# Optimization experiments

Hardware: AMD Instinct MI355X
Metric: run time of the kernel (lower is better)

Reference implementation:

```python
import jax, jax.numpy as jnp
import numpy as np

N = 65536   # voxels
K = 27      # 3x3x3 kernel offsets
LOG_P = float(np.log(101.0))  # Hmax = log(num img channels)
EPS_BN = 1e-5


def bn(x, p):
    # p: [4, C] = (gamma, beta, running_mean, running_var); eval-mode batchnorm
    g, b, m, v = p[0], p[1], p[2], p[3]
    return g * (x - m) * jax.lax.rsqrt(v + EPS_BN) + b


def spconv(x, nbr, W):
    # sparse 3^3 conv as gather-GEMM: x [N,Cin], nbr [N,K] int, W [K,Cin,Cout]
    g = x[nbr]                       # [N, K, Cin] irregular gather
    return jnp.einsum('nkc,kcd->nd', g, W)


def setup_inputs() -> dict:
    key = jax.random.key(0)
    ks = jax.random.split(key, 24)
    inp = {
        'feats': jax.random.uniform(ks[0], (N, 105), dtype=jnp.float32),
        'nbr1': jax.random.randint(ks[1], (N, K), 0, N, dtype=jnp.int32),
        'nbr2': jax.random.randint(ks[2], (N, K), 0, N, dtype=jnp.int32),
        'w_rgb': jax.random.normal(ks[3], (4, 32), jnp.float32) * 0.1,
        'b_rgb': jax.random.normal(ks[4], (32,), jnp.float32) * 0.1,
        'bn_rgb': jax.random.uniform(ks[5], (4, 32), dtype=jnp.float32),
        'w_img': jax.random.normal(ks[6], (101, 32), jnp.float32) * 0.1,
        'b_img': jax.random.normal(ks[7], (32,), jnp.float32) * 0.1,
        'bn_img': jax.random.uniform(ks[8], (4, 32), dtype=jnp.float32),
        'w_e1': jax.random.normal(ks[9], (K, 64, 96), jnp.float32) * 0.05,
        'w_e2': jax.random.normal(ks[10], (K, 96, 96), jnp.float32) * 0.05,
        'bn_e1': jax.random.uniform(ks[11], (4, 96), dtype=jnp.float32),
        'bn_e2': jax.random.uniform(ks[12], (4, 96), dtype=jnp.float32),
        'w_lab': jax.random.normal(ks[13], (96, 19), jnp.float32) * 0.1,
        'w_unlab': jax.random.normal(ks[14], (5, 96, 5), jnp.float32) * 0.1,
        'w_over': jax.random.normal(ks[15], (5, 96, 15), jnp.float32) * 0.1,
        'w_clip1': jax.random.normal(ks[16], (96, 256), jnp.float32) * 0.1,
        'b_clip1': jax.random.normal(ks[17], (256,), jnp.float32) * 0.1,
        'bn_clip': jax.random.uniform(ks[18], (4, 256), dtype=jnp.float32),
        'w_clip2': jax.random.normal(ks[19], (256, 512), jnp.float32) * 0.1,
        'b_clip2': jax.random.normal(ks[20], (512,), jnp.float32) * 0.1,
    }
    return inp


def reference(feats, nbr1, nbr2, w_rgb, b_rgb, bn_rgb, w_img, b_img, bn_img,
              w_e1, w_e2, bn_e1, bn_e2, w_lab, w_unlab, w_over,
              w_clip1, b_clip1, bn_clip, w_clip2, b_clip2):
    rgbi = feats[:, :4]
    p = feats[:, 4:]
    # entropy gate (computed under no_grad in the original)
    p_safe = jnp.clip(p, 1e-12, None)
    H = -(p_safe * jnp.log(p_safe)).sum(axis=1, keepdims=True)
    w = jax.lax.stop_gradient(1.0 - H / LOG_P)
    p_gate = p * w  # eval mode: no dropout
    # 1x1 sparse convs = per-voxel matmuls
    rgb32 = jax.nn.relu(bn(rgbi @ w_rgb + b_rgb, bn_rgb))
    img32 = jax.nn.relu(bn(p_gate @ w_img + b_img, bn_img))
    x = jnp.concatenate([rgb32, img32], axis=1)  # [N, 64]
    # encoder: gather-GEMM sparse 3^3 convs (MinkUNet body pattern), 64->96->96
    x = jax.nn.relu(bn(spconv(x, nbr1, w_e1), bn_e1))
    x = jax.nn.relu(bn(spconv(x, nbr2, w_e2), bn_e2))  # [N, 96] = feats
    # prototype heads (1x1 convs, bias-free)
    logits_lab = x @ w_lab                                 # [N, 19]
    logits_unlab = jnp.einsum('nc,hcp->hnp', x, w_unlab)   # [5, N, 5]
    logits_over = jnp.einsum('nc,hcp->hnp', x, w_over)     # [5, N, 15]
    # clip projector
    h = jax.nn.relu(bn(x @ w_clip1 + b_clip1, bn_clip))
    clip_feats = h @ w_clip2 + b_clip2                     # [N, 512]
    return (logits_lab, logits_unlab, logits_over, x, clip_feats)
```

## Files before the change

kernel.cpp:

```cpp
#include <hip/hip_runtime.h>
#include <math.h>

#define NNODES 65536
#define KNBR 27
#define EPS_BN 1e-5f
#define LOG_P 4.6151205168412597f

typedef float f32x4 __attribute__((ext_vector_type(4)));
typedef short s16x8 __attribute__((ext_vector_type(8)));

__device__ __forceinline__ unsigned short f2bf(float f) {
    union { float f; unsigned int u; } v; v.f = f;
    unsigned int u = v.u;
    unsigned int r = (u + 0x7fffu + ((u >> 16) & 1u)) >> 16;
    return (unsigned short)r;
}

__device__ __forceinline__ void gload16(const void* g, void* l) {
    __builtin_amdgcn_global_load_lds(
        (const __attribute__((address_space(1))) void*)g,
        (__attribute__((address_space(3))) void*)l, 16, 0, 0);
}

__global__ __launch_bounds__(256) void prep_w_kernel(
    const float* __restrict__ W, unsigned short* __restrict__ wpre, int CIN, int NCH)
{
    const int idx = blockIdx.x * 256 + threadIdx.x;
    const int total = KNBR * 96 * NCH * 8;
    if (idx >= total) return;
    const int e  = idx & 7;
    const int t1 = idx >> 3;
    const int ci = t1 % NCH;
    const int t2 = t1 / NCH;
    const int r  = t2 % 96;
    const int k  = t2 / 96;
    const int cc  = ci ^ (r & (NCH - 1));
    const int cin = cc * 8 + e;
    float v = (cin < CIN) ? W[((size_t)k * CIN + cin) * 96 + r] : 0.f;
    wpre[idx] = f2bf(v);
}

__global__ __launch_bounds__(256) void prep_wc1h_kernel(
    const float* __restrict__ w_clip1, const float* __restrict__ w_lab,
    const float* __restrict__ w_unlab, const float* __restrict__ w_over,
    unsigned short* __restrict__ out)
{
    const int idx = blockIdx.x * 256 + threadIdx.x;
    if (idx >= 3 * 384 * 32) return;
    const int e   = idx & 7;
    const int p2  = (idx >> 3) & 3;
    const int col = (idx >> 5) % 384;
    const int kt  = (idx >> 5) / 384;
    const int cin = (kt * 4 + (p2 ^ ((col >> 2) & 3))) * 8 + e;
    float v;
    if (col < 256)      v = w_clip1[(size_t)cin * 256 + col];
    else if (col < 275) v = w_lab[(size_t)cin * 19 + (col - 256)];
    else if (col < 300) { int jj = col - 275, hh = jj / 5,  p = jj - hh * 5;  v = w_unlab[((size_t)hh * 96 + cin) * 5  + p]; }
    else if (col < 375) { int jj = col - 300, hh = jj / 15, p = jj - hh * 15; v = w_over [((size_t)hh * 96 + cin) * 15 + p]; }
    else v = 0.f;
    out[idx] = f2bf(v);
}

__global__ __launch_bounds__(256) void prep_wc2_kernel(
    const float* __restrict__ w_clip2, unsigned short* __restrict__ out)
{
    const int idx = blockIdx.x * 256 + threadIdx.x;
    const int e   = idx & 7;
    const int p2  = (idx >> 3) & 3;
    const int col = (idx >> 5) & 511;
    const int kt  = idx >> 14;
    const int cin = (kt * 4 + (p2 ^ ((col >> 2) & 3))) * 8 + e;
    out[idx] = f2bf(w_clip2[(size_t)cin * 512 + col]);
}

__global__ __launch_bounds__(256) void stage1_kernel(
    const float* __restrict__ feats,
    const float* __restrict__ w_rgb, const float* __restrict__ b_rgb, const float* __restrict__ bn_rgb,
    const float* __restrict__ w_img, const float* __restrict__ b_img, const float* __restrict__ bn_img,
    unsigned short* __restrict__ x64b)
{
    __shared__ float s_f[4][106];
    const int wid  = threadIdx.x >> 6;
    const int lane = threadIdx.x & 63;
    const int n = blockIdx.x * 4 + wid;
    const float* fr = feats + (size_t)n * 105;
    for (int i = lane; i < 105; i += 64) s_f[wid][i] = fr[i];
    __syncthreads();

    float s = 0.f;
    for (int i = lane; i < 101; i += 64) {
        float pv = s_f[wid][4 + i];
        float ps = fmaxf(pv, 1e-12f);
        s += ps * logf(ps);
    }
    #pragma unroll
    for (int off = 32; off > 0; off >>= 1) s += __shfl_xor(s, off, 64);
    const float wgt = 1.0f + s * (1.0f / LOG_P);

    if (lane < 32) {
        const int j = lane;
        float acc = b_rgb[j];
        #pragma unroll
        for (int c = 0; c < 4; ++c) acc += s_f[wid][c] * w_rgb[c*32 + j];
        float y = bn_rgb[j] * (acc - bn_rgb[64+j]) * rsqrtf(bn_rgb[96+j] + EPS_BN) + bn_rgb[32+j];
        x64b[(size_t)n*64 + j] = f2bf(fmaxf(y, 0.f));
    } else {
        const int j = lane - 32;
        float acc = 0.f;
        for (int c = 0; c < 101; ++c) acc += s_f[wid][4+c] * w_img[c*32 + j];
        acc = acc * wgt + b_img[j];
        float y = bn_img[j] * (acc - bn_img[64+j]) * rsqrtf(bn_img[96+j] + EPS_BN) + bn_img[32+j];
        x64b[(size_t)n*64 + 32 + j] = f2bf(fmaxf(y, 0.f));
    }
}

template<int CIN, bool OUTBF>
__global__ __launch_bounds__(256, 2) void spconv_mfma(
    const char* __restrict__ xinb,
    const int*  __restrict__ nbr,
    const char* __restrict__ wpre,
    const float* __restrict__ bnp,
    float* __restrict__ outf,
    unsigned short* __restrict__ outb)
{
    constexpr int KT   = CIN / 32;
    constexpr int NCH  = (CIN == 96) ? 16 : 8;
    constexpr int CM   = NCH - 1;
    constexpr int ROWB = NCH * 16;
    constexpr int STG  = (96 * ROWB) / 4096;

    __shared__ int s_nbr[128 * KNBR];
    __shared__ __align__(16) char s_b[2][96 * ROWB];

    const int t   = threadIdx.x;
    const int wid = t >> 6;
    const int l   = t & 63;
    const int l15 = l & 15;
    const int l4  = l >> 4;
    const int n0  = blockIdx.x * 128;

    for (int i = t; i < 128 * KNBR; i += 256) s_nbr[i] = nbr[(size_t)n0 * KNBR + i];

    f32x4 acc[2][6];
    #pragma unroll
    for (int mt = 0; mt < 2; ++mt)
        #pragma unroll
        for (int nt = 0; nt < 6; ++nt) acc[mt][nt] = (f32x4){0.f, 0.f, 0.f, 0.f};

    s16x8 a0[2][KT], a1[2][KT], a2r[2][KT];

#define STAGE(kk) do {                                                         \
    const char* _src = wpre + (size_t)(kk) * (96 * ROWB);                      \
    char* _dst = &s_b[(kk) & 1][0];                                            \
    _Pragma("unroll")                                                          \
    for (int _i = 0; _i < STG; ++_i)                                           \
        gload16(_src + _i * 4096 + t * 16, _dst + _i * 4096 + (wid << 10));    \
    asm volatile("" ::: "memory");                                             \
} while (0)

#define PRE(areg, kk) do {                                                     \
    _Pragma("unroll")                                                          \
    for (int _mt = 0; _mt < 2; ++_mt) {                                        \
        const int _nb = s_nbr[(wid * 32 + _mt * 16 + l15) * KNBR + (kk)];      \
        const char* _rp = xinb + (size_t)_nb * (CIN * 2) + (l4 << 4);          \
        _Pragma("unroll")                                                      \
        for (int _kt = 0; _kt < KT; ++_kt)                                     \
            areg[_mt][_kt] = *(const s16x8*)(_rp + _kt * 64);                  \
    }                                                                          \
} while (0)

#define COMP(areg, kk) do {                                                    \
    const char* _bb = &s_b[(kk) & 1][0];                                       \
    _Pragma("unroll")                                                          \
    for (int _kt = 0; _kt < KT; ++_kt) {                                       \
        s16x8 _bf[6];                                                          \
        _Pragma("unroll")                                                      \
        for (int _nt = 0; _nt < 6; ++_nt) {                                    \
            const int _row = _nt * 16 + l15;                                   \
            const int _c   = _kt * 4 + l4;                                     \
            _bf[_nt] = *(const s16x8*)(_bb + _row * ROWB + ((_c ^ (_row & CM)) << 4)); \
        }                                                                      \
        _Pragma("unroll")                                                      \
        for (int _nt = 0; _nt < 6; ++_nt) {                                    \
            acc[0][_nt] = __builtin_amdgcn_mfma_f32_16x16x32_bf16(areg[0][_kt], _bf[_nt], acc[0][_nt], 0, 0, 0); \
            acc[1][_nt] = __builtin_amdgcn_mfma_f32_16x16x32_bf16(areg[1][_kt], _bf[_nt], acc[1][_nt], 0, 0, 0); \
        }                                                                      \
    }                                                                          \
} while (0)

#define KBAR() do {                                                            \
    if (KT == 3) asm volatile("s_waitcnt vmcnt(6)" ::: "memory");              \
    else         asm volatile("s_waitcnt vmcnt(4)" ::: "memory");              \
    __builtin_amdgcn_s_barrier();                                              \
} while (0)

    __syncthreads();
    PRE(a0, 0);
    PRE(a1, 1);
    STAGE(0);
    __syncthreads();

    for (int k = 0; k < 24; k += 3) {
        STAGE(k + 1);
        PRE(a2r, k + 2);
        COMP(a0, k);
        KBAR();
        STAGE(k + 2);
        PRE(a0, k + 3);
        COMP(a1, k + 1);
        KBAR();
        STAGE(k + 3);
        PRE(a1, k + 4);
        COMP(a2r, k + 2);
        KBAR();
    }
    STAGE(25);
    PRE(a2r, 26);
    COMP(a0, 24);
    KBAR();
    STAGE(26);
    COMP(a1, 25);
    asm volatile("s_waitcnt vmcnt(0)" ::: "memory");
    __builtin_amdgcn_s_barrier();
    COMP(a2r, 26);

#undef STAGE
#undef PRE
#undef COMP
#undef KBAR

    #pragma unroll
    for (int mt = 0; mt < 2; ++mt)
        #pragma unroll
        for (int nt = 0; nt < 6; ++nt) {
            const int d = nt * 16 + l15;
            const float sc = bnp[d] * rsqrtf(bnp[288 + d] + EPS_BN);
            const float mb = bnp[192 + d];
            const float bb = bnp[96 + d];
            #pragma unroll
            for (int q = 0; q < 4; ++q) {
                const int node = n0 + wid * 32 + mt * 16 + l4 * 4 + q;
                float y = sc * (acc[mt][nt][q] - mb) + bb;
                y = fmaxf(y, 0.f);
                if (OUTBF) outb[(size_t)node * 96 + d] = f2bf(y);
                else       outf[(size_t)node * 96 + d] = y;
            }
        }
}

__global__ __launch_bounds__(512, 2) void fused_clip_heads(
    const float* __restrict__ x,
    const char* __restrict__ wc1h,
    const char* __restrict__ wc2,
    const float* __restrict__ b_clip1, const float* __restrict__ bn_clip,
    const float* __restrict__ b_clip2,
    float* __restrict__ out_lab, float* __restrict__ out_unlab, float* __restrict__ out_over,
    float* __restrict__ outc)
{
    extern __shared__ __align__(16) char lds[];
    char* reg0 = lds;
    char* s_h  = lds + 65536;

    const int t   = threadIdx.x;
    const int wid = t >> 6;
    const int l   = t & 63;
    const int l15 = l & 15;
    const int l4  = l >> 4;
    const int wm  = wid >> 2;
    const int wn  = wid & 3;
    const int r0  = blockIdx.x * 128;

#define STG1(kt) do {                                                          \
    const char* _s = wc1h + (size_t)(kt) * 24576;                              \
    char* _d = reg0 + ((kt) & 1) * 32768;                                      \
    _Pragma("unroll")                                                          \
    for (int _i = 0; _i < 3; ++_i)                                             \
        gload16(_s + _i * 8192 + t * 16, _d + _i * 8192 + (wid << 10));        \
} while (0)

#define STG2(kt) do {                                                          \
    const char* _s = wc2 + (size_t)(kt) * 32768;                               \
    char* _d = reg0 + ((kt) & 1) * 32768;                                      \
    _Pragma("unroll")                                                          \
    for (int _i = 0; _i < 4; ++_i)                                             \
        gload16(_s + _i * 8192 + t * 16, _d + _i * 8192 + (wid << 10));        \
} while (0)

    STG1(0);

    s16x8 af[3][4];
    #pragma unroll
    for (int kt = 0; kt < 3; ++kt)
        #pragma unroll
        for (int mt = 0; mt < 4; ++mt) {
            const int r = r0 + wm*64 + mt*16 + l15;
            const float* bp = x + (size_t)r*96 + kt*32 + l4*8;
            const float4 xa = *(const float4*)bp;
            const float4 xb = *(const float4*)(bp + 4);
            s16x8 v;
            v[0]=(short)f2bf(xa.x); v[1]=(short)f2bf(xa.y); v[2]=(short)f2bf(xa.z); v[3]=(short)f2bf(xa.w);
            v[4]=(short)f2bf(xb.x); v[5]=(short)f2bf(xb.y); v[6]=(short)f2bf(xb.z); v[7]=(short)f2bf(xb.w);
            af[kt][mt] = v;
        }

    f32x4 acc1[4][6];
    #pragma unroll
    for (int mt = 0; mt < 4; ++mt)
        #pragma unroll
        for (int nt = 0; nt < 6; ++nt) acc1[mt][nt] = (f32x4){0.f,0.f,0.f,0.f};

    __syncthreads();

    for (int kt = 0; kt < 3; ++kt) {
        if (kt < 2) STG1(kt + 1);
        const char* buf = reg0 + (kt & 1) * 32768;
        s16x8 bf[6];
        #pragma unroll
        for (int nt = 0; nt < 6; ++nt) {
            const int col = wn*96 + nt*16 + l15;
            bf[nt] = *(const s16x8*)(buf + col*64 + ((l4 ^ ((col >> 2) & 3)) << 4));
        }
        #pragma unroll
        for (int nt = 0; nt < 6; ++nt)
            #pragma unroll
            for (int mt = 0; mt < 4; ++mt)
                acc1[mt][nt] = __builtin_amdgcn_mfma_f32_16x16x32_bf16(af[kt][mt], bf[nt], acc1[mt][nt], 0, 0, 0);
        __syncthreads();
    }

    STG2(0);

    #pragma unroll
    for (int nt = 0; nt < 6; ++nt) {
        const int j = wn*96 + nt*16 + l15;
        if (j < 256) {
            const float sc = bn_clip[j] * rsqrtf(bn_clip[768 + j] + EPS_BN);
            const float mb = bn_clip[512 + j];
            const float bb = bn_clip[256 + j];
            const float bias = b_clip1[j];
            const int c = j >> 3, e = j & 7;
            #pragma unroll
            for (int mt = 0; mt < 4; ++mt)
                #pragma unroll
                for (int q = 0; q < 4; ++q) {
                    const int row = wm*64 + mt*16 + l4*4 + q;
                    float y = fmaxf(sc * (acc1[mt][nt][q] + bias - mb) + bb, 0.f);
                    *(unsigned short*)(s_h + row*512 + ((c ^ (row & 31)) << 4) + e*2) = f2bf(y);
                }
        } else if (j < 375) {
            const int jh = j - 256;
            #pragma unroll
            for (int mt = 0; mt < 4; ++mt)
                #pragma unroll
                for (int q = 0; q < 4; ++q) {
                    const int n = r0 + wm*64 + mt*16 + l4*4 + q;
                    const float v = acc1[mt][nt][q];
                    if (jh < 19)      out_lab[(size_t)n*19 + jh] = v;
                    else if (jh < 44) { int jj = jh-19, hh = jj/5,  p = jj-hh*5;  out_unlab[((size_t)hh*NNODES + n)*5  + p] = v; }
                    else              { int jj = jh-44, hh = jj/15, p = jj-hh*15; out_over [((size_t)hh*NNODES + n)*15 + p] = v; }
                }
        }
    }
    __syncthreads();

    f32x4 acc2[4][8];
    #pragma unroll
    for (int mt = 0; mt < 4; ++mt)
        #pragma unroll
        for (int nt = 0; nt < 8; ++nt) acc2[mt][nt] = (f32x4){0.f,0.f,0.f,0.f};

    for (int kt = 0; kt < 8; ++kt) {
        if (kt < 7) STG2(kt + 1);
        const char* buf = reg0 + (kt & 1) * 32768;
        s16x8 a2[4];
        #pragma unroll
        for (int mt = 0; mt < 4; ++mt) {
            const int row = wm*64 + mt*16 + l15;
            a2[mt] = *(const s16x8*)(s_h + row*512 + (((kt*4 + l4) ^ (row & 31)) << 4));
        }
        s16x8 b2[8];
        #pragma unroll
        for (int nt = 0; nt < 8; ++nt) {
            const int col = wn*128 + nt*16 + l15;
            b2[nt] = *(const s16x8*)(buf + col*64 + ((l4 ^ ((col >> 2) & 3)) << 4));
        }
        #pragma unroll
        for (int nt = 0; nt < 8; ++nt)
            #pragma unroll
            for (int mt = 0; mt < 4; ++mt)
                acc2[mt][nt] = __builtin_amdgcn_mfma_f32_16x16x32_bf16(a2[mt], b2[nt], acc2[mt][nt], 0, 0, 0);
        __syncthreads();
    }
#undef STG1
#undef STG2

    #pragma unroll
    for (int nt = 0; nt < 8; ++nt) {
        const int col = wn*128 + nt*16 + l15;
        const float bb = b_clip2[col];
        #pragma unroll
        for (int mt = 0; mt < 4; ++mt)
            #pragma unroll
            for (int q = 0; q < 4; ++q) {
                const int row = wm*64 + mt*16 + l4*4 + q;
                outc[(size_t)(r0 + row)*512 + col] = acc2[mt][nt][q] + bb;
            }
    }
}

extern "C" void kernel_launch(void* const* d_in, const int* in_sizes, int n_in,
                              void* d_out, int out_size, void* d_ws, size_t ws_size,
                              hipStream_t stream)
{
    const float* feats   = (const float*)d_in[0];
    const int*   nbr1    = (const int*)  d_in[1];
    const int*   nbr2    = (const int*)  d_in[2];
    const float* w_rgb   = (const float*)d_in[3];
    const float* b_rgb   = (const float*)d_in[4];
    const float* bn_rgb  = (const float*)d_in[5];
    const float* w_img   = (const float*)d_in[6];
    const float* b_img   = (const float*)d_in[7];
    const float* bn_img  = (const float*)d_in[8];
    const float* w_e1    = (const float*)d_in[9];
    const float* w_e2    = (const float*)d_in[10];
    const float* bn_e1   = (const float*)d_in[11];
    const float* bn_e2   = (const float*)d_in[12];
    const float* w_lab   = (const float*)d_in[13];
    const float* w_unlab = (const float*)d_in[14];
    const float* w_over  = (const float*)d_in[15];
    const float* w_clip1 = (const float*)d_in[16];
    const float* b_clip1 = (const float*)d_in[17];
    const float* bn_clip = (const float*)d_in[18];
    const float* w_clip2 = (const float*)d_in[19];
    const float* b_clip2 = (const float*)d_in[20];

    float* out = (float*)d_out;
    const size_t off_unlab = (size_t)NNODES * 19;
    const size_t off_over  = (size_t)NNODES * 44;
    const size_t off_x     = (size_t)NNODES * 119;
    const size_t off_clip  = (size_t)NNODES * 215;

    char* scratch = (char*)(out + off_clip);
    unsigned short* x64b  = (unsigned short*)scratch;
    unsigned short* x96b  = (unsigned short*)(scratch + (8u << 20));
    unsigned short* wpre1 = (unsigned short*)(scratch + (21u << 20));
    unsigned short* wpre2 = (unsigned short*)(scratch + (22u << 20));

    char* wc1h = (char*)d_ws;
    char* wc2  = (char*)d_ws + 73728;

    prep_w_kernel<<<(KNBR*96*8*8  + 255) / 256, 256, 0, stream>>>(w_e1, wpre1, 64, 8);
    prep_w_kernel<<<(KNBR*96*16*8 + 255) / 256, 256, 0, stream>>>(w_e2, wpre2, 96, 16);
    prep_wc1h_kernel<<<(3*384*32 + 255) / 256, 256, 0, stream>>>(w_clip1, w_lab, w_unlab, w_over,
                                                                 (unsigned short*)wc1h);
    prep_wc2_kernel<<<131072 / 256, 256, 0, stream>>>(w_clip2, (unsigned short*)wc2);

    stage1_kernel<<<NNODES/4, 256, 0, stream>>>(feats, w_rgb, b_rgb, bn_rgb, w_img, b_img, bn_img, x64b);

    spconv_mfma<64, true ><<<NNODES/128, 256, 0, stream>>>((const char*)x64b, nbr1, (const char*)wpre1,
                                                           bn_e1, nullptr, x96b);
    spconv_mfma<96, false><<<NNODES/128, 256, 0, stream>>>((const char*)x96b, nbr2, (const char*)wpre2,
                                                           bn_e2, out + off_x, nullptr);

    fused_clip_heads<<<NNODES/128, 512, 131072, stream>>>(
        out + off_x, wc1h, wc2, b_clip1, bn_clip, b_clip2,
        out, out + off_unlab, out + off_over, out + off_clip);
}
```

Measured before the change: 241.4 us.

## Merge weight prep kernels and halve clip-head tile to raise occupancy

After: 236.4 us (median of 2 runs). -2.1%, faster.

```diff
diff --git a/kernel.cpp b/kernel.cpp
--- a/kernel.cpp
+++ b/kernel.cpp
@@ -22,55 +22,51 @@
         (__attribute__((address_space(3))) void*)l, 16, 0, 0);
 }
 
-__global__ __launch_bounds__(256) void prep_w_kernel(
-    const float* __restrict__ W, unsigned short* __restrict__ wpre, int CIN, int NCH)
-{
-    const int idx = blockIdx.x * 256 + threadIdx.x;
-    const int total = KNBR * 96 * NCH * 8;
-    if (idx >= total) return;
-    const int e  = idx & 7;
-    const int t1 = idx >> 3;
-    const int ci = t1 % NCH;
-    const int t2 = t1 / NCH;
-    const int r  = t2 % 96;
-    const int k  = t2 / 96;
-    const int cc  = ci ^ (r & (NCH - 1));
-    const int cin = cc * 8 + e;
-    float v = (cin < CIN) ? W[((size_t)k * CIN + cin) * 96 + r] : 0.f;
-    wpre[idx] = f2bf(v);
-}
-
-__global__ __launch_bounds__(256) void prep_wc1h_kernel(
+__global__ __launch_bounds__(256) void prep_all_kernel(
+    const float* __restrict__ w_e1, const float* __restrict__ w_e2,
     const float* __restrict__ w_clip1, const float* __restrict__ w_lab,
     const float* __restrict__ w_unlab, const float* __restrict__ w_over,
-    unsigned short* __restrict__ out)
+    const float* __restrict__ w_clip2,
+    unsigned short* __restrict__ wpre1, unsigned short* __restrict__ wpre2,
+    unsigned short* __restrict__ wc1h, unsigned short* __restrict__ wc2)
 {
-    const int idx = blockIdx.x * 256 + threadIdx.x;
-    if (idx >= 3 * 384 * 32) return;
-    const int e   = idx & 7;
-    const int p2  = (idx >> 3) & 3;
-    const int col = (idx >> 5) % 384;
-    const int kt  = (idx >> 5) / 384;
-    const int cin = (kt * 4 + (p2 ^ ((col >> 2) & 3))) * 8 + e;
-    float v;
-    if (col < 256)      v = w_clip1[(size_t)cin * 256 + col];
-    else if (col < 275) v = w_lab[(size_t)cin * 19 + (col - 256)];
-    else if (col < 300) { int jj = col - 275, hh = jj / 5,  p = jj - hh * 5;  v = w_unlab[((size_t)hh * 96 + cin) * 5  + p]; }
-    else if (col < 375) { int jj = col - 300, hh = jj / 15, p = jj - hh * 15; v = w_over [((size_t)hh * 96 + cin) * 15 + p]; }
-    else v = 0.f;
-    out[idx] = f2bf(v);
-}
-
-__global__ __launch_bounds__(256) void prep_wc2_kernel(
-    const float* __restrict__ w_clip2, unsigned short* __restrict__ out)
-{
-    const int idx = blockIdx.x * 256 + threadIdx.x;
-    const int e   = idx & 7;
-    const int p2  = (idx >> 3) & 3;
-    const int col = (idx >> 5) & 511;
-    const int kt  = idx >> 14;
-    const int cin = (kt * 4 + (p2 ^ ((col >> 2) & 3))) * 8 + e;
-    out[idx] = f2bf(w_clip2[(size_t)cin * 512 + col]);
+    const int N1 = KNBR*96*8*8;
+    const int N2 = KNBR*96*16*8;
+    const int N3 = 3*384*32;
+    const int N4 = 8*512*32;
+    int idx = blockIdx.x * 256 + threadIdx.x;
+    if (idx < N1) {
+        const int e = idx & 7, ci = (idx >> 3) & 7, r = (idx >> 6) % 96, k = (idx >> 6) / 96;
+        const int cin = (ci ^ (r & 7)) * 8 + e;
+        wpre1[idx] = f2bf(w_e1[((size_t)k*64 + cin)*96 + r]);
+        return;
+    }
+    idx -= N1;
+    if (idx < N2) {
+        const int e = idx & 7, ci = (idx >> 3) & 15, r = (idx >> 7) % 96, k = (idx >> 7) / 96;
+        const int cin = (ci ^ (r & 15)) * 8 + e;
+        wpre2[idx] = f2bf(w_e2[((size_t)k*96 + cin)*96 + r]);
+        return;
+    }
+    idx -= N2;
+    if (idx < N3) {
+        const int e = idx & 7, p2 = (idx >> 3) & 3, col = (idx >> 5) % 384, kt = (idx >> 5) / 384;
+        const int cin = (kt*4 + (p2 ^ ((col >> 2) & 3)))*8 + e;
+        float v;
+        if (col < 256)      v = w_clip1[(size_t)cin*256 + col];
+        else if (col < 275) v = w_lab[(size_t)cin*19 + (col - 256)];
+        else if (col < 300) { int jj = col-275, hh = jj/5,  p = jj-hh*5;  v = w_unlab[((size_t)hh*96 + cin)*5  + p]; }
+        else if (col < 375) { int jj = col-300, hh = jj/15, p = jj-hh*15; v = w_over [((size_t)hh*96 + cin)*15 + p]; }
+        else v = 0.f;
+        wc1h[idx] = f2bf(v);
+        return;
+    }
+    idx -= N3;
+    if (idx < N4) {
+        const int e = idx & 7, p2 = (idx >> 3) & 3, col = (idx >> 5) & 511, kt = idx >> 14;
+        const int cin = (kt*4 + (p2 ^ ((col >> 2) & 3)))*8 + e;
+        wc2[idx] = f2bf(w_clip2[(size_t)cin*512 + col]);
+    }
 }
 
 __global__ __launch_bounds__(256) void stage1_kernel(
@@ -248,7 +244,7 @@
         }
 }
 
-__global__ __launch_bounds__(512, 2) void fused_clip_heads(
+__global__ __launch_bounds__(512, 4) void fused_clip_heads(
     const float* __restrict__ x,
     const char* __restrict__ wc1h,
     const char* __restrict__ wc2,
@@ -259,7 +255,7 @@
 {
     extern __shared__ __align__(16) char lds[];
     char* reg0 = lds;
-    char* s_h  = lds + 65536;
+    char* s_h  = lds + 32768;
 
     const int t   = threadIdx.x;
     const int wid = t >> 6;
@@ -268,32 +264,28 @@
     const int l4  = l >> 4;
     const int wm  = wid >> 2;
     const int wn  = wid & 3;
-    const int r0  = blockIdx.x * 128;
+    const int r0  = blockIdx.x * 64;
 
 #define STG1(kt) do {                                                          \
     const char* _s = wc1h + (size_t)(kt) * 24576;                              \
-    char* _d = reg0 + ((kt) & 1) * 32768;                                      \
     _Pragma("unroll")                                                          \
     for (int _i = 0; _i < 3; ++_i)                                             \
-        gload16(_s + _i * 8192 + t * 16, _d + _i * 8192 + (wid << 10));        \
+        gload16(_s + _i * 8192 + t * 16, reg0 + _i * 8192 + (wid << 10));      \
 } while (0)
 
 #define STG2(kt) do {                                                          \
     const char* _s = wc2 + (size_t)(kt) * 32768;                               \
-    char* _d = reg0 + ((kt) & 1) * 32768;                                      \
     _Pragma("unroll")                                                          \
     for (int _i = 0; _i < 4; ++_i)                                             \
-        gload16(_s + _i * 8192 + t * 16, _d + _i * 8192 + (wid << 10));        \
-} while (0)
-
-    STG1(0);
-
-    s16x8 af[3][4];
+        gload16(_s + _i * 8192 + t * 16, reg0 + _i * 8192 + (wid << 10));      \
+} while (0)
+
+    s16x8 af[3][2];
     #pragma unroll
     for (int kt = 0; kt < 3; ++kt)
         #pragma unroll
-        for (int mt = 0; mt < 4; ++mt) {
-            const int r = r0 + wm*64 + mt*16 + l15;
+        for (int mt = 0; mt < 2; ++mt) {
+            const int r = r0 + wm*32 + mt*16 + l15;
             const float* bp = x + (size_t)r*96 + kt*32 + l4*8;
             const float4 xa = *(const float4*)bp;
             const float4 xb = *(const float4*)(bp + 4);
@@ -303,27 +295,25 @@
             af[kt][mt] = v;
         }
 
-    f32x4 acc1[4][6];
-    #pragma unroll
-    for (int mt = 0; mt < 4; ++mt)
+    f32x4 acc1[2][6];
+    #pragma unroll
+    for (int mt = 0; mt < 2; ++mt)
         #pragma unroll
         for (int nt = 0; nt < 6; ++nt) acc1[mt][nt] = (f32x4){0.f,0.f,0.f,0.f};
 
-    __syncthreads();
-
     for (int kt = 0; kt < 3; ++kt) {
-        if (kt < 2) STG1(kt + 1);
-        const char* buf = reg0 + (kt & 1) * 32768;
+        STG1(kt);
+        __syncthreads();
         s16x8 bf[6];
         #pragma unroll
         for (int nt = 0; nt < 6; ++nt) {
             const int col = wn*96 + nt*16 + l15;
-            bf[nt] = *(const s16x8*)(buf + col*64 + ((l4 ^ ((col >> 2) & 3)) << 4));
+            bf[nt] = *(const s16x8*)(reg0 + col*64 + ((l4 ^ ((col >> 2) & 3)) << 4));
         }
         #pragma unroll
         for (int nt = 0; nt < 6; ++nt)
             #pragma unroll
-            for (int mt = 0; mt < 4; ++mt)
+            for (int mt = 0; mt < 2; ++mt)
                 acc1[mt][nt] = __builtin_amdgcn_mfma_f32_16x16x32_bf16(af[kt][mt], bf[nt], acc1[mt][nt], 0, 0, 0);
         __syncthreads();
     }
@@ -340,20 +330,20 @@
             const float bias = b_clip1[j];
             const int c = j >> 3, e = j & 7;
             #pragma unroll
-            for (int mt = 0; mt < 4; ++mt)
+            for (int mt = 0; mt < 2; ++mt)
                 #pragma unroll
                 for (int q = 0; q < 4; ++q) {
-                    const int row = wm*64 + mt*16 + l4*4 + q;
+                    const int row = wm*32 + mt*16 + l4*4 + q;
                     float y = fmaxf(sc * (acc1[mt][nt][q] + bias - mb) + bb, 0.f);
                     *(unsigned short*)(s_h + row*512 + ((c ^ (row & 31)) << 4) + e*2) = f2bf(y);
                 }
         } else if (j < 375) {
             const int jh = j - 256;
             #pragma unroll
-            for (int mt = 0; mt < 4; ++mt)
+            for (int mt = 0; mt < 2; ++mt)
                 #pragma unroll
                 for (int q = 0; q < 4; ++q) {
-                    const int n = r0 + wm*64 + mt*16 + l4*4 + q;
+                    const int n = r0 + wm*32 + mt*16 + l4*4 + q;
                     const float v = acc1[mt][nt][q];
                     if (jh < 19)      out_lab[(size_t)n*19 + jh] = v;
                     else if (jh < 44) { int jj = jh-19, hh = jj/5,  p = jj-hh*5;  out_unlab[((size_t)hh*NNODES + n)*5  + p] = v; }
@@ -363,33 +353,35 @@
     }
     __syncthreads();
 
-    f32x4 acc2[4][8];
-    #pragma unroll
-    for (int mt = 0; mt < 4; ++mt)
+    f32x4 acc2[2][8];
+    #pragma unroll
+    for (int mt = 0; mt < 2; ++mt)
         #pragma unroll
         for (int nt = 0; nt < 8; ++nt) acc2[mt][nt] = (f32x4){0.f,0.f,0.f,0.f};
 
     for (int kt = 0; kt < 8; ++kt) {
-        if (kt < 7) STG2(kt + 1);
-        const char* buf = reg0 + (kt & 1) * 32768;
-        s16x8 a2[4];
-        #pragma unroll
-        for (int mt = 0; mt < 4; ++mt) {
-            const int row = wm*64 + mt*16 + l15;
+        s16x8 a2[2];
+        #pragma unroll
+        for (int mt = 0; mt < 2; ++mt) {
+            const int row = wm*32 + mt*16 + l15;
             a2[mt] = *(const s16x8*)(s_h + row*512 + (((kt*4 + l4) ^ (row & 31)) << 4));
         }
         s16x8 b2[8];
         #pragma unroll
         for (int nt = 0; nt < 8; ++nt) {
             const int col = wn*128 + nt*16 + l15;
-            b2[nt] = *(const s16x8*)(buf + col*64 + ((l4 ^ ((col >> 2) & 3)) << 4));
+            b2[nt] = *(const s16x8*)(reg0 + col*64 + ((l4 ^ ((col >> 2) & 3)) << 4));
         }
         #pragma unroll
         for (int nt = 0; nt < 8; ++nt)
             #pragma unroll
-            for (int mt = 0; mt < 4; ++mt)
+            for (int mt = 0; mt < 2; ++mt)
                 acc2[mt][nt] = __builtin_amdgcn_mfma_f32_16x16x32_bf16(a2[mt], b2[nt], acc2[mt][nt], 0, 0, 0);
         __syncthreads();
+        if (kt < 7) {
+            STG2(kt + 1);
+            __syncthreads();
+        }
     }
 #undef STG1
 #undef STG2
@@ -399,10 +391,10 @@
         const int col = wn*128 + nt*16 + l15;
         const float bb = b_clip2[col];
         #pragma unroll
-        for (int mt = 0; mt < 4; ++mt)
+        for (int mt = 0; mt < 2; ++mt)
             #pragma unroll
             for (int q = 0; q < 4; ++q) {
-                const int row = wm*64 + mt*16 + l4*4 + q;
+                const int row = wm*32 + mt*16 + l4*4 + q;
                 outc[(size_t)(r0 + row)*512 + col] = acc2[mt][nt][q] + bb;
             }
     }
@@ -449,11 +441,10 @@
     char* wc1h = (char*)d_ws;
     char* wc2  = (char*)d_ws + 73728;
 
-    prep_w_kernel<<<(KNBR*96*8*8  + 255) / 256, 256, 0, stream>>>(w_e1, wpre1, 64, 8);
-    prep_w_kernel<<<(KNBR*96*16*8 + 255) / 256, 256, 0, stream>>>(w_e2, wpre2, 96, 16);
-    prep_wc1h_kernel<<<(3*384*32 + 255) / 256, 256, 0, stream>>>(w_clip1, w_lab, w_unlab, w_over,
-                                                                 (unsigned short*)wc1h);
-    prep_wc2_kernel<<<131072 / 256, 256, 0, stream>>>(w_clip2, (unsigned short*)wc2);
+    const int NPREP = KNBR*96*8*8 + KNBR*96*16*8 + 3*384*32 + 8*512*32;
+    prep_all_kernel<<<(NPREP + 255) / 256, 256, 0, stream>>>(
+        w_e1, w_e2, w_clip1, w_lab, w_unlab, w_over, w_clip2,
+        wpre1, wpre2, (unsigned short*)wc1h, (unsigned short*)wc2);
 
     stage1_kernel<<<NNODES/4, 256, 0, stream>>>(feats, w_rgb, b_rgb, bn_rgb, w_img, b_img, bn_img, x64b);
 
@@ -462,7 +453,7 @@
     spconv_mfma<96, false><<<NNODES/128, 256, 0, stream>>>((const char*)x96b, nbr2, (const char*)wpre2,
                                                            bn_e2, out + off_x, nullptr);
 
-    fused_clip_heads<<<NNODES/128, 512, 131072, stream>>>(
+    fused_clip_heads<<<NNODES/64, 512, 65536, stream>>>(
         out + off_x, wc1h, wc2, b_clip1, bn_clip, b_clip2,
         out, out + off_unlab, out + off_over, out + off_clip);
 }
```
